# Optimization experiments

Measured on AMD Instinct MI355X. Metric: run time of the kernel, lower is better.

Reference implementation:

```python
import jax, jax.numpy as jnp
import numpy as np

N, IN_DIM, D, H, OUT = 4096, 512, 256, 256, 128


def setup_inputs() -> dict:
    key = jax.random.key(0)
    ks = jax.random.split(key, 12)
    s = 0.05
    x = jax.random.normal(ks[0], (N, IN_DIM), dtype=jnp.float32)
    # sparse-ish dense adjacency mask (avg degree ~80), int since only adj>0 is used
    adj = (jax.random.uniform(ks[1], (N, N)) < 0.02).astype(jnp.int32)
    return {
        "x": x,
        "adj": adj,
        "lin1_w": jax.random.normal(ks[2], (D, IN_DIM), dtype=jnp.float32) * s,
        "lin1_b": jax.random.normal(ks[3], (D,), dtype=jnp.float32) * s,
        "gat_W": jax.random.normal(ks[4], (D, D), dtype=jnp.float32) * s,
        "a_self": jax.random.normal(ks[5], (D,), dtype=jnp.float32) * s,
        "a_neigh": jax.random.normal(ks[6], (D,), dtype=jnp.float32) * s,
        "W_ih": jax.random.normal(ks[7], (4 * H, D), dtype=jnp.float32) * s,
        "W_hh": jax.random.normal(ks[8], (4 * H, H), dtype=jnp.float32) * s,
        "lin2_w": jax.random.normal(ks[9], (OUT, D), dtype=jnp.float32) * s,
        "lin2_b": jax.random.normal(ks[10], (OUT,), dtype=jnp.float32) * s,
    }


def reference(x, adj, lin1_w, lin1_b, gat_W, a_self, a_neigh, W_ih, W_hh, lin2_w, lin2_b):
    M = jnp.float32(0.2)        # scalar M passed by EWNELayer
    LRELU_SLOPE = 0.2           # alpha given to GraphAttentionLayer
    NEG_INF = jnp.float32(-9e15)

    # lin1
    x1 = x @ lin1_w.T + lin1_b                       # [N, D]

    # --- GraphAttentionLayer (DAEGC-style, dense adjacency mask) ---
    h = x1 @ gat_W                                   # [N, D]
    e = (h @ a_self)[:, None] + (h @ a_neigh)[None, :]  # [N, N]
    e = jax.nn.leaky_relu(e * M, LRELU_SLOPE)
    scores = jnp.where(adj > 0, e, NEG_INF)
    attn = jax.nn.softmax(scores, axis=1)            # [N, N]
    h_prime = attn @ h                               # [N, D]
    g = jnp.tanh(jax.nn.elu(h_prime))                # ELU (concat=True) then tanh

    # --- single-timestep LSTM, no bias, h0 = c0 = 0 ---
    h0 = jnp.zeros((N, H), dtype=g.dtype)
    c0 = jnp.zeros((N, H), dtype=g.dtype)
    gates = g @ W_ih.T + h0 @ W_hh.T                 # [N, 4H], torch order i,f,g,o
    i_g, f_g, g_g, o_g = jnp.split(gates, 4, axis=1)
    i_g = jax.nn.sigmoid(i_g)
    f_g = jax.nn.sigmoid(f_g)
    g_g = jnp.tanh(g_g)
    o_g = jax.nn.sigmoid(o_g)
    c1 = f_g * c0 + i_g * g_g
    h1 = o_g * jnp.tanh(c1)                          # [N, H]

    # lin2 -> normalize -> dot-product decode
    out = h1 @ lin2_w.T + lin2_b                     # [N, OUT]
    norm = jnp.maximum(jnp.linalg.norm(out, axis=1, keepdims=True), 1e-12)
    z = out / norm
    A_pred = jax.nn.sigmoid(z @ z.T)                 # [N, N]
    return A_pred, z, out
```

## Files before the change

kernel.cpp:

```cpp
#include <hip/hip_runtime.h>

#define NN_ 4096
#define IN_DIM_ 512
#define D_ 256
#define OUT_ 128

typedef unsigned short u16;
typedef unsigned int u32;
typedef __attribute__((ext_vector_type(8))) short short8;
typedef __attribute__((ext_vector_type(4))) float f32x4;

union U16x8 { uint4 u4; short8 s8; };

__device__ __forceinline__ u16 f2bf(float f){
  u32 u = __builtin_bit_cast(u32, f);
  u = (u + 0x7FFFu + ((u >> 16) & 1u)) >> 16;
  return (u16)u;
}
__device__ __forceinline__ float bf2f(u16 u){ return __builtin_bit_cast(float, ((u32)u) << 16); }
__device__ __forceinline__ float sigm(float v){ return __fdividef(1.f, 1.f + __expf(-v)); }

__device__ __forceinline__ void mfma_mainloop(const u16* __restrict__ A,
    const u16* __restrict__ B, int K, int ldA, int ldB, int row0, int col0,
    uint4* As, uint4* Bs, f32x4 acc[4][4], int tid) {
  const int wave = tid >> 6, lane = tid & 63;
  const int wm = wave >> 1, wn = wave & 1;
  const int r16 = lane & 15, kg = lane >> 4;
  for (int k0 = 0; k0 < K; k0 += 64) {
    #pragma unroll
    for (int i = 0; i < 4; i++) {
      int id = tid + (i << 8);
      int r = id >> 3, cc = id & 7;
      As[(r << 3) + (cc ^ (r & 7))] = *(const uint4*)(A + (size_t)(row0 + r) * ldA + k0 + cc * 8);
      Bs[(r << 3) + (cc ^ (r & 7))] = *(const uint4*)(B + (size_t)(col0 + r) * ldB + k0 + cc * 8);
    }
    __syncthreads();
    #pragma unroll
    for (int ks = 0; ks < 2; ks++) {
      int kb = (ks << 2) + kg;
      U16x8 a[4], b[4];
      #pragma unroll
      for (int m2 = 0; m2 < 4; m2++) {
        int r = (wm << 6) + (m2 << 4) + r16;
        a[m2].u4 = As[(r << 3) + (kb ^ (r & 7))];
      }
      #pragma unroll
      for (int n2 = 0; n2 < 4; n2++) {
        int r = (wn << 6) + (n2 << 4) + r16;
        b[n2].u4 = Bs[(r << 3) + (kb ^ (r & 7))];
      }
      #pragma unroll
      for (int m2 = 0; m2 < 4; m2++)
        #pragma unroll
        for (int n2 = 0; n2 < 4; n2++)
          acc[m2][n2] = __builtin_amdgcn_mfma_f32_16x16x32_bf16(
              a[m2].s8, b[n2].s8, acc[m2][n2], 0, 0, 0);
    }
    __syncthreads();
  }
}

__global__ __launch_bounds__(256) void prep_kernel(
    const float* __restrict__ lin1_w, const float* __restrict__ gat_W,
    const float* __restrict__ lin1_b,
    u16* __restrict__ WcT_bf, float* __restrict__ bcomb) {
  __shared__ __align__(16) float sh[2 * 32 * 68];
  const int b = blockIdx.x, tid = threadIdx.x;
  if (b < 32) {
    float (*As)[68] = (float(*)[68])sh;
    float (*Bs)[68] = (float(*)[68])(sh + 32 * 68);
    int m0 = (b & 7) << 6, n0 = (b >> 3) << 6;
    const int tx = tid & 15, ty = tid >> 4;
    float acc[4][4] = {};
    for (int k0 = 0; k0 < 256; k0 += 32) {
      #pragma unroll
      for (int i = 0; i < 2; i++) {
        int id = tid + (i << 8);
        int kk = id >> 4, c4 = (id & 15) << 2;
        *(float4*)&As[kk][c4] = *(const float4*)(lin1_w + (size_t)(k0 + kk) * 512 + m0 + c4);
        *(float4*)&Bs[kk][c4] = *(const float4*)(gat_W + (size_t)(k0 + kk) * 256 + n0 + c4);
      }
      __syncthreads();
      #pragma unroll
      for (int kk = 0; kk < 32; kk++) {
        float4 av = *(const float4*)&As[kk][ty << 2];
        float4 bv = *(const float4*)&Bs[kk][tx << 2];
        float a_[4] = {av.x, av.y, av.z, av.w};
        float b_[4] = {bv.x, bv.y, bv.z, bv.w};
        #pragma unroll
        for (int r = 0; r < 4; r++)
          #pragma unroll
          for (int c = 0; c < 4; c++)
            acc[r][c] = __builtin_fmaf(a_[r], b_[c], acc[r][c]);
      }
      __syncthreads();
    }
    #pragma unroll
    for (int r = 0; r < 4; r++)
      #pragma unroll
      for (int c = 0; c < 4; c++)
        WcT_bf[(size_t)(n0 + (tx << 2) + c) * 512 + m0 + (ty << 2) + r] = f2bf(acc[r][c]);
  } else {
    float a = 0.f;
    #pragma unroll 8
    for (int d = 0; d < 256; d++)
      a = __builtin_fmaf(lin1_b[d], gat_W[(size_t)d * 256 + tid], a);
    bcomb[tid] = a;
  }
}

__global__ __launch_bounds__(256) void hgemm_st_kernel(const float* __restrict__ x,
    const u16* __restrict__ WcT, const float* __restrict__ bias,
    const float* __restrict__ a_self, const float* __restrict__ a_nei,
    const float* __restrict__ W_ih, const float* __restrict__ lin2_w,
    u16* __restrict__ h_bf, float* __restrict__ s, float* __restrict__ t,
    u16* __restrict__ Wih_bf, u16* __restrict__ l2w_bf) {
  __shared__ uint4 As[16 * 8];
  __shared__ uint4 Bs[256 * 8];
  __shared__ float sred[4][16];
  __shared__ float tred[4][16];
  const int tid = threadIdx.x;
  int b = blockIdx.x;
  if (b >= 256) {
    b -= 256;
    if (b < 256) {
      int r = (b << 2) + (tid >> 6);
      int grp = r >> 6, gate = (r >> 4) & 3, hcl = r & 15;
      int orig = gate * 256 + grp * 16 + hcl;
      int k = (tid & 63) << 2;
      float4 v = *(const float4*)(W_ih + (size_t)orig * 256 + k);
      ushort4 o = {f2bf(v.x), f2bf(v.y), f2bf(v.z), f2bf(v.w)};
      *(ushort4*)(Wih_bf + (size_t)r * 256 + k) = o;
    } else {
      int off = (b - 256) * 1024 + tid * 4;
      float4 v = *(const float4*)(lin2_w + off);
      ushort4 o = {f2bf(v.x), f2bf(v.y), f2bf(v.z), f2bf(v.w)};
      *(ushort4*)(l2w_bf + off) = o;
    }
    return;
  }
  const int row0 = b << 4;
  const int wave = tid >> 6, lane = tid & 63;
  const int r16 = lane & 15, kg = lane >> 4;
  f32x4 acc[4];
  #pragma unroll
  for (int n2 = 0; n2 < 4; n2++) acc[n2] = (f32x4){0.f,0.f,0.f,0.f};
  for (int k0 = 0; k0 < IN_DIM_; k0 += 64) {
    if (tid < 128) {
      int r = tid >> 3, cc = tid & 7;
      const float* src = x + (size_t)(row0 + r) * IN_DIM_ + k0 + cc * 8;
      float4 lo = *(const float4*)src;
      float4 hi = *(const float4*)(src + 4);
      u16 e[8] = {f2bf(lo.x), f2bf(lo.y), f2bf(lo.z), f2bf(lo.w),
                  f2bf(hi.x), f2bf(hi.y), f2bf(hi.z), f2bf(hi.w)};
      As[(r << 3) + (cc ^ (r & 7))] = *(uint4*)e;
    }
    #pragma unroll
    for (int i = 0; i < 8; i++) {
      int id = tid + (i << 8);
      int r = id >> 3, cc = id & 7;
      Bs[(r << 3) + (cc ^ (r & 7))] = *(const uint4*)(WcT + (size_t)r * IN_DIM_ + k0 + cc * 8);
    }
    __syncthreads();
    #pragma unroll
    for (int ks = 0; ks < 2; ks++) {
      int kb = (ks << 2) + kg;
      U16x8 a, bb[4];
      a.u4 = As[(r16 << 3) + (kb ^ (r16 & 7))];
      #pragma unroll
      for (int n2 = 0; n2 < 4; n2++) {
        int r = (wave << 6) + (n2 << 4) + r16;
        bb[n2].u4 = Bs[(r << 3) + (kb ^ (r & 7))];
      }
      #pragma unroll
      for (int n2 = 0; n2 < 4; n2++)
        acc[n2] = __builtin_amdgcn_mfma_f32_16x16x32_bf16(a.s8, bb[n2].s8, acc[n2], 0, 0, 0);
    }
    __syncthreads();
  }
  float ps[4] = {0.f,0.f,0.f,0.f}, pt[4] = {0.f,0.f,0.f,0.f};
  #pragma unroll
  for (int n2 = 0; n2 < 4; n2++) {
    int col = (wave << 6) + (n2 << 4) + r16;
    float as = a_self[col], an = a_nei[col], bs = bias[col];
    #pragma unroll
    for (int q = 0; q < 4; q++) {
      float v = acc[n2][q] + bs;
      h_bf[(size_t)(row0 + (kg << 2) + q) * D_ + col] = f2bf(v);
      ps[q] = __builtin_fmaf(v, as, ps[q]);
      pt[q] = __builtin_fmaf(v, an, pt[q]);
    }
  }
  #pragma unroll
  for (int q = 0; q < 4; q++) {
    #pragma unroll
    for (int off = 8; off; off >>= 1) {
      ps[q] += __shfl_xor(ps[q], off);
      pt[q] += __shfl_xor(pt[q], off);
    }
  }
  if (r16 == 0) {
    #pragma unroll
    for (int q = 0; q < 4; q++) {
      sred[wave][(kg << 2) + q] = ps[q];
      tred[wave][(kg << 2) + q] = pt[q];
    }
  }
  __syncthreads();
  if (tid < 16)
    s[row0 + tid] = sred[0][tid] + sred[1][tid] + sred[2][tid] + sred[3][tid];
  else if (tid < 32)
    t[row0 + tid - 16] = tred[0][tid-16] + tred[1][tid-16] + tred[2][tid-16] + tred[3][tid-16];
}

#define MAXN 512
__global__ __launch_bounds__(256) void attn3_kernel(const int* __restrict__ adj,
    const u16* __restrict__ h_bf, const float* __restrict__ s,
    const float* __restrict__ t, u16* __restrict__ g_bf) {
  __shared__ int nidx[MAXN];
  __shared__ float ne[MAXN];
  __shared__ float red[4][256];
  __shared__ int wtot[4];
  __shared__ float reds[4];
  const int tid = threadIdx.x;
  const int row = blockIdx.x;
  const int lane = tid & 63, wave = tid >> 6;
  const int4* arow = (const int4*)(adj + (size_t)row * NN_);
  int4 a4[4];
  #pragma unroll
  for (int i = 0; i < 4; i++) a4[i] = arow[(i << 8) + tid];
  int vals[16] = {a4[0].x, a4[0].y, a4[0].z, a4[0].w, a4[1].x, a4[1].y, a4[1].z, a4[1].w,
                  a4[2].x, a4[2].y, a4[2].z, a4[2].w, a4[3].x, a4[3].y, a4[3].z, a4[3].w};
  int c = 0;
  #pragma unroll
  for (int q = 0; q < 16; q++) c += (vals[q] > 0);
  int pref = c;
  #pragma unroll
  for (int off = 1; off < 64; off <<= 1) {
    int u = __shfl_up(pref, off);
    if (lane >= off) pref += u;
  }
  if (lane == 63) wtot[wave] = pref;
  __syncthreads();
  int woff = 0;
  #pragma unroll
  for (int w = 0; w < 4; w++) woff += (w < wave) ? wtot[w] : 0;
  int n = wtot[0] + wtot[1] + wtot[2] + wtot[3];
  float si = s[row];
  int p = woff + pref - c;
  float ls = 0.f;
  #pragma unroll
  for (int i = 0; i < 4; i++)
    #pragma unroll
    for (int q = 0; q < 4; q++) {
      if (vals[(i << 2) + q] > 0) {
        int j = (i << 10) + (tid << 2) + q;
        float e = 0.2f * (si + t[j]);
        e = e > 0.f ? e : 0.2f * e;
        float wgt = __expf(e);
        if (p < MAXN) { nidx[p] = j; ne[p] = wgt; ls += wgt; }
        p++;
      }
    }
  if (n > MAXN) n = MAXN;
  #pragma unroll
  for (int off = 32; off; off >>= 1) ls += __shfl_xor(ls, off);
  if (lane == 0) reds[wave] = ls;
  __syncthreads();
  float S = reds[0] + reds[1] + reds[2] + reds[3];
  const int hl = lane & 31, ksel = lane >> 5;
  float acc[8] = {0.f, 0.f, 0.f, 0.f, 0.f, 0.f, 0.f, 0.f};
  #pragma unroll 4
  for (int k = (wave << 1) + ksel; k < n; k += 8) {
    float wgt = ne[k];
    int j = nidx[k];
    U16x8 hv; hv.u4 = *(const uint4*)(h_bf + ((size_t)j << 8) + (hl << 3));
    #pragma unroll
    for (int q = 0; q < 8; q++)
      acc[q] = __builtin_fmaf(wgt, bf2f((u16)hv.s8[q]), acc[q]);
  }
  #pragma unroll
  for (int q = 0; q < 8; q++) acc[q] += __shfl_down(acc[q], 32);
  if (lane < 32) {
    #pragma unroll
    for (int q = 0; q < 8; q++) red[wave][(hl << 3) + q] = acc[q];
  }
  __syncthreads();
  float hp;
  if (n > 0) {
    hp = (red[0][tid] + red[1][tid] + red[2][tid] + red[3][tid]) / S;
  } else {
    float a2 = 0.f;
    for (int j = 0; j < NN_; j++) a2 += bf2f(h_bf[((size_t)j << 8) + tid]);
    hp = a2 / NN_;
  }
  float el = hp > 0.f ? hp : __expf(hp) - 1.f;
  g_bf[((size_t)row << 8) + tid] = f2bf(tanhf(el));
}

__global__ __launch_bounds__(256) void gates_lstm_kernel(const u16* __restrict__ A,
    const u16* __restrict__ B, u16* __restrict__ h1b) {
  __shared__ uint4 As[128 * 8];
  __shared__ uint4 Bs[128 * 8];
  const int tid = threadIdx.x;
  const int row0 = blockIdx.y << 7, col0 = blockIdx.x << 7;
  f32x4 acc[4][4];
  #pragma unroll
  for (int m2 = 0; m2 < 4; m2++)
    #pragma unroll
    for (int n2 = 0; n2 < 4; n2++) acc[m2][n2] = (f32x4){0.f,0.f,0.f,0.f};
  mfma_mainloop(A, B, D_, D_, D_, row0, col0, As, Bs, acc, tid);
  const int wave = tid >> 6, lane = tid & 63;
  const int r16 = lane & 15, kg = lane >> 4;
  const int orow = row0 + ((wave >> 1) << 6);
  const int hc = ((blockIdx.x << 1) + (wave & 1)) * 16 + r16;
  #pragma unroll
  for (int m2 = 0; m2 < 4; m2++)
    #pragma unroll
    for (int q = 0; q < 4; q++) {
      size_t grow = orow + (m2 << 4) + (kg << 2) + q;
      float ig = acc[m2][0][q], gg = acc[m2][2][q], og = acc[m2][3][q];
      float c1 = sigm(ig) * tanhf(gg);
      h1b[grow * D_ + hc] = f2bf(sigm(og) * tanhf(c1));
    }
}

__global__ __launch_bounds__(256) void lin2f_kernel(const u16* __restrict__ A,
    const u16* __restrict__ B, const float* __restrict__ bias,
    float* __restrict__ out, float* __restrict__ z, u16* __restrict__ zb) {
  __shared__ uint4 As[16 * 8];
  __shared__ uint4 Bs[128 * 8];
  __shared__ float ssred[4][16];
  const int tid = threadIdx.x;
  const int wave = tid >> 6, lane = tid & 63;
  const int r16 = lane & 15, kg = lane >> 4;
  const int row0 = blockIdx.x << 4;
  f32x4 acc[2];
  acc[0] = (f32x4){0.f,0.f,0.f,0.f}; acc[1] = (f32x4){0.f,0.f,0.f,0.f};
  for (int k0 = 0; k0 < D_; k0 += 64) {
    if (tid < 128) {
      int r = tid >> 3, cc = tid & 7;
      As[(r << 3) + (cc ^ (r & 7))] = *(const uint4*)(A + (size_t)(row0 + r) * D_ + k0 + cc * 8);
    }
    #pragma unroll
    for (int i = 0; i < 4; i++) {
      int id = tid + (i << 8);
      int r = id >> 3, cc = id & 7;
      Bs[(r << 3) + (cc ^ (r & 7))] = *(const uint4*)(B + (size_t)r * D_ + k0 + cc * 8);
    }
    __syncthreads();
    #pragma unroll
    for (int ks = 0; ks < 2; ks++) {
      int kb = (ks << 2) + kg;
      U16x8 a, bb[2];
      a.u4 = As[(r16 << 3) + (kb ^ (r16 & 7))];
      #pragma unroll
      for (int n2 = 0; n2 < 2; n2++) {
        int r = (wave << 5) + (n2 << 4) + r16;
        bb[n2].u4 = Bs[(r << 3) + (kb ^ (r & 7))];
      }
      #pragma unroll
      for (int n2 = 0; n2 < 2; n2++)
        acc[n2] = __builtin_amdgcn_mfma_f32_16x16x32_bf16(a.s8, bb[n2].s8, acc[n2], 0, 0, 0);
    }
    __syncthreads();
  }
  float v[2][4], ss[4];
  #pragma unroll
  for (int q = 0; q < 4; q++) ss[q] = 0.f;
  #pragma unroll
  for (int n2 = 0; n2 < 2; n2++) {
    int col = (wave << 5) + (n2 << 4) + r16;
    float bs = bias[col];
    #pragma unroll
    for (int q = 0; q < 4; q++) {
      float vv = acc[n2][q] + bs;
      v[n2][q] = vv;
      ss[q] = __builtin_fmaf(vv, vv, ss[q]);
    }
  }
  #pragma unroll
  for (int q = 0; q < 4; q++)
    #pragma unroll
    for (int off = 8; off; off >>= 1) ss[q] += __shfl_xor(ss[q], off);
  if (r16 == 0) {
    #pragma unroll
    for (int q = 0; q < 4; q++) ssred[wave][(kg << 2) + q] = ss[q];
  }
  __syncthreads();
  #pragma unroll
  for (int q = 0; q < 4; q++) {
    int rrow = (kg << 2) + q;
    float tot = ssred[0][rrow] + ssred[1][rrow] + ssred[2][rrow] + ssred[3][rrow];
    float inv = __fdividef(1.f, fmaxf(sqrtf(tot), 1e-12f));
    size_t grow = row0 + rrow;
    #pragma unroll
    for (int n2 = 0; n2 < 2; n2++) {
      int col = (wave << 5) + (n2 << 4) + r16;
      float vv = v[n2][q], zz = vv * inv;
      out[grow * OUT_ + col] = vv;
      z[grow * OUT_ + col] = zz;
      zb[grow * OUT_ + col] = f2bf(zz);
    }
  }
}

__global__ __launch_bounds__(256) void decode_kernel(const u16* __restrict__ zb,
    float* __restrict__ C) {
  __shared__ uint4 As[128 * 8];
  __shared__ uint4 Bs[128 * 8];
  const int tid = threadIdx.x;
  const int row0 = blockIdx.y << 7, col0 = blockIdx.x << 7;
  f32x4 acc[4][4];
  #pragma unroll
  for (int m2 = 0; m2 < 4; m2++)
    #pragma unroll
    for (int n2 = 0; n2 < 4; n2++) acc[m2][n2] = (f32x4){0.f,0.f,0.f,0.f};
  mfma_mainloop(zb, zb, OUT_, OUT_, OUT_, row0, col0, As, Bs, acc, tid);
  const int wave = tid >> 6, lane = tid & 63;
  const int r16 = lane & 15, kg = lane >> 4;
  const int orow = row0 + ((wave >> 1) << 6), ocol = col0 + ((wave & 1) << 6);
  #pragma unroll
  for (int m2 = 0; m2 < 4; m2++)
    #pragma unroll
    for (int n2 = 0; n2 < 4; n2++)
      #pragma unroll
      for (int q = 0; q < 4; q++) {
        size_t gr = orow + (m2 << 4) + (kg << 2) + q;
        int gc = ocol + (n2 << 4) + r16;
        C[gr * NN_ + gc] = sigm(acc[m2][n2][q]);
      }
}

extern "C" void kernel_launch(void* const* d_in, const int* in_sizes, int n_in,
                              void* d_out, int out_size, void* d_ws, size_t ws_size,
                              hipStream_t stream) {
  const float* x      = (const float*)d_in[0];
  const int*   adj    = (const int*)  d_in[1];
  const float* lin1_w = (const float*)d_in[2];
  const float* lin1_b = (const float*)d_in[3];
  const float* gat_W  = (const float*)d_in[4];
  const float* a_self = (const float*)d_in[5];
  const float* a_nei  = (const float*)d_in[6];
  const float* W_ih   = (const float*)d_in[7];
  const float* lin2_w = (const float*)d_in[9];
  const float* lin2_b = (const float*)d_in[10];

  float* A_pred = (float*)d_out;
  float* z_out  = A_pred + (size_t)NN_ * NN_;
  float* out_o  = z_out + (size_t)NN_ * OUT_;

  char* w = (char*)d_ws;
  u16* h_bf   = (u16*)w;
  u16* g_bf   = (u16*)(w + (2u << 20));
  u16* h1_bf  = (u16*)(w + (4u << 20));
  u16* zb     = (u16*)(w + (6u << 20));
  u16* Wih_bf = (u16*)(w + (7u << 20));
  u16* WcT_bf = (u16*)(w + (7u << 20) + (512u << 10));
  u16* l2w_bf = (u16*)(w + (7u << 20) + (768u << 10));
  float* bcomb= (float*)(w + (7u << 20) + (832u << 10));
  float* s    = (float*)(w + (7u << 20) + (896u << 10));
  float* t    = (float*)(w + (7u << 20) + (960u << 10));

  prep_kernel<<<dim3(33), dim3(256), 0, stream>>>(
      lin1_w, gat_W, lin1_b, WcT_bf, bcomb);
  hgemm_st_kernel<<<dim3(544), dim3(256), 0, stream>>>(
      x, WcT_bf, bcomb, a_self, a_nei, W_ih, lin2_w, h_bf, s, t, Wih_bf, l2w_bf);
  attn3_kernel<<<dim3(4096), dim3(256), 0, stream>>>(adj, h_bf, s, t, g_bf);
  gates_lstm_kernel<<<dim3(8, 32), dim3(256), 0, stream>>>(g_bf, Wih_bf, h1_bf);
  lin2f_kernel<<<dim3(256), dim3(256), 0, stream>>>(h1_bf, l2w_bf, lin2_b, out_o, z_out, zb);
  decode_kernel<<<dim3(32, 32), dim3(256), 0, stream>>>(zb, A_pred);
}
```

Baseline: 87.19 us.

## Drop unused forget-gate GEMM columns, shrink prep tiles, vectorize t loads

Because c0 is zero, the forget gate never affects the output, so the W_ih repack now keeps only the i, g and o gate rows. The gates GEMM uses 96-column tiles with a 4x3 MFMA layout, cutting a quarter of its FLOPs and B-tile loads. The prep kernel switches to 32x32 tiles over 128 blocks to spread the small weight-fusion GEMM across more CUs. The attention kernel preloads t as vector loads instead of scattered scalar loads per neighbour. Risks include lower MFMA efficiency from the odd tile shape and more workspace-offset bookkeeping.

```diff
diff --git a/kernel.cpp b/kernel.cpp
--- a/kernel.cpp
+++ b/kernel.cpp
@@ -64,42 +64,35 @@
     const float* __restrict__ lin1_w, const float* __restrict__ gat_W,
     const float* __restrict__ lin1_b,
     u16* __restrict__ WcT_bf, float* __restrict__ bcomb) {
-  __shared__ __align__(16) float sh[2 * 32 * 68];
+  __shared__ __align__(16) float As[32][36];
+  __shared__ __align__(16) float Bs[32][36];
   const int b = blockIdx.x, tid = threadIdx.x;
-  if (b < 32) {
-    float (*As)[68] = (float(*)[68])sh;
-    float (*Bs)[68] = (float(*)[68])(sh + 32 * 68);
-    int m0 = (b & 7) << 6, n0 = (b >> 3) << 6;
+  if (b < 128) {
+    const int m0 = (b & 15) << 5;
+    const int n0 = (b >> 4) << 5;
     const int tx = tid & 15, ty = tid >> 4;
-    float acc[4][4] = {};
+    float acc[2][2] = {};
     for (int k0 = 0; k0 < 256; k0 += 32) {
-      #pragma unroll
-      for (int i = 0; i < 2; i++) {
-        int id = tid + (i << 8);
-        int kk = id >> 4, c4 = (id & 15) << 2;
-        *(float4*)&As[kk][c4] = *(const float4*)(lin1_w + (size_t)(k0 + kk) * 512 + m0 + c4);
-        *(float4*)&Bs[kk][c4] = *(const float4*)(gat_W + (size_t)(k0 + kk) * 256 + n0 + c4);
-      }
+      int kk = tid >> 3, c4 = (tid & 7) << 2;
+      *(float4*)&As[kk][c4] = *(const float4*)(lin1_w + (size_t)(k0 + kk) * 512 + m0 + c4);
+      *(float4*)&Bs[kk][c4] = *(const float4*)(gat_W + (size_t)(k0 + kk) * 256 + n0 + c4);
       __syncthreads();
       #pragma unroll
-      for (int kk = 0; kk < 32; kk++) {
-        float4 av = *(const float4*)&As[kk][ty << 2];
-        float4 bv = *(const float4*)&Bs[kk][tx << 2];
-        float a_[4] = {av.x, av.y, av.z, av.w};
-        float b_[4] = {bv.x, bv.y, bv.z, bv.w};
-        #pragma unroll
-        for (int r = 0; r < 4; r++)
-          #pragma unroll
-          for (int c = 0; c < 4; c++)
-            acc[r][c] = __builtin_fmaf(a_[r], b_[c], acc[r][c]);
+      for (int k2 = 0; k2 < 32; k2++) {
+        float a0 = As[k2][(ty << 1)], a1 = As[k2][(ty << 1) + 1];
+        float b0 = Bs[k2][(tx << 1)], b1 = Bs[k2][(tx << 1) + 1];
+        acc[0][0] = __builtin_fmaf(a0, b0, acc[0][0]);
+        acc[0][1] = __builtin_fmaf(a0, b1, acc[0][1]);
+        acc[1][0] = __builtin_fmaf(a1, b0, acc[1][0]);
+        acc[1][1] = __builtin_fmaf(a1, b1, acc[1][1]);
       }
       __syncthreads();
     }
     #pragma unroll
-    for (int r = 0; r < 4; r++)
-      #pragma unroll
-      for (int c = 0; c < 4; c++)
-        WcT_bf[(size_t)(n0 + (tx << 2) + c) * 512 + m0 + (ty << 2) + r] = f2bf(acc[r][c]);
+    for (int r = 0; r < 2; r++)
+      #pragma unroll
+      for (int c = 0; c < 2; c++)
+        WcT_bf[(size_t)(n0 + (tx << 1) + c) * 512 + m0 + (ty << 1) + r] = f2bf(acc[r][c]);
   } else {
     float a = 0.f;
     #pragma unroll 8
@@ -114,7 +107,7 @@
     const float* __restrict__ a_self, const float* __restrict__ a_nei,
     const float* __restrict__ W_ih, const float* __restrict__ lin2_w,
     u16* __restrict__ h_bf, float* __restrict__ s, float* __restrict__ t,
-    u16* __restrict__ Wih_bf, u16* __restrict__ l2w_bf) {
+    u16* __restrict__ Wihp_bf, u16* __restrict__ l2w_bf) {
   __shared__ uint4 As[16 * 8];
   __shared__ uint4 Bs[256 * 8];
   __shared__ float sred[4][16];
@@ -123,16 +116,18 @@
   int b = blockIdx.x;
   if (b >= 256) {
     b -= 256;
-    if (b < 256) {
+    if (b < 192) {
       int r = (b << 2) + (tid >> 6);
-      int grp = r >> 6, gate = (r >> 4) & 3, hcl = r & 15;
+      int grp = r / 48, rem = r - grp * 48;
+      int gidx = rem >> 4, hcl = rem & 15;
+      int gate = (gidx == 0) ? 0 : ((gidx == 1) ? 2 : 3);
       int orig = gate * 256 + grp * 16 + hcl;
       int k = (tid & 63) << 2;
       float4 v = *(const float4*)(W_ih + (size_t)orig * 256 + k);
       ushort4 o = {f2bf(v.x), f2bf(v.y), f2bf(v.z), f2bf(v.w)};
-      *(ushort4*)(Wih_bf + (size_t)r * 256 + k) = o;
+      *(ushort4*)(Wihp_bf + (size_t)r * 256 + k) = o;
     } else {
-      int off = (b - 256) * 1024 + tid * 4;
+      int off = (b - 192) * 1024 + tid * 4;
       float4 v = *(const float4*)(lin2_w + off);
       ushort4 o = {f2bf(v.x), f2bf(v.y), f2bf(v.z), f2bf(v.w)};
       *(ushort4*)(l2w_bf + off) = o;
@@ -231,6 +226,9 @@
   for (int i = 0; i < 4; i++) a4[i] = arow[(i << 8) + tid];
   int vals[16] = {a4[0].x, a4[0].y, a4[0].z, a4[0].w, a4[1].x, a4[1].y, a4[1].z, a4[1].w,
                   a4[2].x, a4[2].y, a4[2].z, a4[2].w, a4[3].x, a4[3].y, a4[3].z, a4[3].w};
+  f32x4 tv[4];
+  #pragma unroll
+  for (int i = 0; i < 4; i++) tv[i] = ((const f32x4*)t)[(i << 8) + tid];
   int c = 0;
   #pragma unroll
   for (int q = 0; q < 16; q++) c += (vals[q] > 0);
@@ -255,7 +253,7 @@
     for (int q = 0; q < 4; q++) {
       if (vals[(i << 2) + q] > 0) {
         int j = (i << 10) + (tid << 2) + q;
-        float e = 0.2f * (si + t[j]);
+        float e = 0.2f * (si + tv[i][q]);
         e = e > 0.f ? e : 0.2f * e;
         float wgt = __expf(e);
         if (p < MAXN) { nidx[p] = j; ne[p] = wgt; ls += wgt; }
@@ -301,25 +299,62 @@
 __global__ __launch_bounds__(256) void gates_lstm_kernel(const u16* __restrict__ A,
     const u16* __restrict__ B, u16* __restrict__ h1b) {
   __shared__ uint4 As[128 * 8];
-  __shared__ uint4 Bs[128 * 8];
+  __shared__ uint4 Bs[96 * 8];
   const int tid = threadIdx.x;
-  const int row0 = blockIdx.y << 7, col0 = blockIdx.x << 7;
-  f32x4 acc[4][4];
+  const int row0 = blockIdx.y << 7;
+  const int col0 = blockIdx.x * 96;
+  const int wave = tid >> 6, lane = tid & 63;
+  const int wm = wave >> 1, wn = wave & 1;
+  const int r16 = lane & 15, kg = lane >> 4;
+  f32x4 acc[4][3];
   #pragma unroll
   for (int m2 = 0; m2 < 4; m2++)
     #pragma unroll
-    for (int n2 = 0; n2 < 4; n2++) acc[m2][n2] = (f32x4){0.f,0.f,0.f,0.f};
-  mfma_mainloop(A, B, D_, D_, D_, row0, col0, As, Bs, acc, tid);
-  const int wave = tid >> 6, lane = tid & 63;
-  const int r16 = lane & 15, kg = lane >> 4;
-  const int orow = row0 + ((wave >> 1) << 6);
-  const int hc = ((blockIdx.x << 1) + (wave & 1)) * 16 + r16;
+    for (int n2 = 0; n2 < 3; n2++) acc[m2][n2] = (f32x4){0.f,0.f,0.f,0.f};
+  for (int k0 = 0; k0 < D_; k0 += 64) {
+    #pragma unroll
+    for (int i = 0; i < 4; i++) {
+      int id = tid + (i << 8);
+      int r = id >> 3, cc = id & 7;
+      As[(r << 3) + (cc ^ (r & 7))] = *(const uint4*)(A + (size_t)(row0 + r) * D_ + k0 + cc * 8);
+    }
+    #pragma unroll
+    for (int i = 0; i < 3; i++) {
+      int id = tid + (i << 8);
+      int r = id >> 3, cc = id & 7;
+      Bs[(r << 3) + (cc ^ (r & 7))] = *(const uint4*)(B + (size_t)(col0 + r) * D_ + k0 + cc * 8);
+    }
+    __syncthreads();
+    #pragma unroll
+    for (int ks = 0; ks < 2; ks++) {
+      int kb = (ks << 2) + kg;
+      U16x8 a[4], bb[3];
+      #pragma unroll
+      for (int m2 = 0; m2 < 4; m2++) {
+        int r = (wm << 6) + (m2 << 4) + r16;
+        a[m2].u4 = As[(r << 3) + (kb ^ (r & 7))];
+      }
+      #pragma unroll
+      for (int n2 = 0; n2 < 3; n2++) {
+        int r = wn * 48 + (n2 << 4) + r16;
+        bb[n2].u4 = Bs[(r << 3) + (kb ^ (r & 7))];
+      }
+      #pragma unroll
+      for (int m2 = 0; m2 < 4; m2++)
+        #pragma unroll
+        for (int n2 = 0; n2 < 3; n2++)
+          acc[m2][n2] = __builtin_amdgcn_mfma_f32_16x16x32_bf16(
+              a[m2].s8, bb[n2].s8, acc[m2][n2], 0, 0, 0);
+    }
+    __syncthreads();
+  }
+  const int hc = ((blockIdx.x << 1) + wn) * 16 + r16;
   #pragma unroll
   for (int m2 = 0; m2 < 4; m2++)
     #pragma unroll
     for (int q = 0; q < 4; q++) {
-      size_t grow = orow + (m2 << 4) + (kg << 2) + q;
-      float ig = acc[m2][0][q], gg = acc[m2][2][q], og = acc[m2][3][q];
+      size_t grow = row0 + (wm << 6) + (m2 << 4) + (kg << 2) + q;
+      float ig = acc[m2][0][q], gg = acc[m2][1][q], og = acc[m2][2][q];
       float c1 = sigm(ig) * tanhf(gg);
       h1b[grow * D_ + hc] = f2bf(sigm(og) * tanhf(c1));
     }
@@ -451,23 +486,23 @@
   float* out_o  = z_out + (size_t)NN_ * OUT_;
 
   char* w = (char*)d_ws;
-  u16* h_bf   = (u16*)w;
-  u16* g_bf   = (u16*)(w + (2u << 20));
-  u16* h1_bf  = (u16*)(w + (4u << 20));
-  u16* zb     = (u16*)(w + (6u << 20));
-  u16* Wih_bf = (u16*)(w + (7u << 20));
-  u16* WcT_bf = (u16*)(w + (7u << 20) + (512u << 10));
-  u16* l2w_bf = (u16*)(w + (7u << 20) + (768u << 10));
-  float* bcomb= (float*)(w + (7u << 20) + (832u << 10));
-  float* s    = (float*)(w + (7u << 20) + (896u << 10));
-  float* t    = (float*)(w + (7u << 20) + (960u << 10));
-
-  prep_kernel<<<dim3(33), dim3(256), 0, stream>>>(
+  u16* h_bf    = (u16*)w;
+  u16* g_bf    = (u16*)(w + (2u << 20));
+  u16* h1_bf   = (u16*)(w + (4u << 20));
+  u16* zb      = (u16*)(w + (6u << 20));
+  u16* Wihp_bf = (u16*)(w + (7u << 20));
+  u16* WcT_bf  = (u16*)(w + (7u << 20) + (384u << 10));
+  u16* l2w_bf  = (u16*)(w + (7u << 20) + (640u << 10));
+  float* bcomb = (float*)(w + (7u << 20) + (704u << 10));
+  float* s     = (float*)(w + (7u << 20) + (768u << 10));
+  float* t     = (float*)(w + (7u << 20) + (832u << 10));
+
+  prep_kernel<<<dim3(129), dim3(256), 0, stream>>>(
       lin1_w, gat_W, lin1_b, WcT_bf, bcomb);
-  hgemm_st_kernel<<<dim3(544), dim3(256), 0, stream>>>(
-      x, WcT_bf, bcomb, a_self, a_nei, W_ih, lin2_w, h_bf, s, t, Wih_bf, l2w_bf);
+  hgemm_st_kernel<<<dim3(480), dim3(256), 0, stream>>>(
+      x, WcT_bf, bcomb, a_self, a_nei, W_ih, lin2_w, h_bf, s, t, Wihp_bf, l2w_bf);
   attn3_kernel<<<dim3(4096), dim3(256), 0, stream>>>(adj, h_bf, s, t, g_bf);
-  gates_lstm_kernel<<<dim3(8, 32), dim3(256), 0, stream>>>(g_bf, Wih_bf, h1_bf);
+  gates_lstm_kernel<<<dim3(8, 32), dim3(256), 0, stream>>>(g_bf, Wihp_bf, h1_bf);
   lin2f_kernel<<<dim3(256), dim3(256), 0, stream>>>(h1_bf, l2w_bf, lin2_b, out_o, z_out, zb);
   decode_kernel<<<dim3(32, 32), dim3(256), 0, stream>>>(zb, A_pred);
 }
```

Result: faster. 81.57 us (-6.4%).
